# Kernel optimization log

Measured on AMD Instinct MI355X. Metric: run time of the kernel, lower is better.

## Reference

```python
import jax, jax.numpy as jnp
import numpy as np

B, H, S, D = 8, 16, 512, 512  # note: module's final matmul requires D == S


def setup_inputs() -> dict:
    key = jax.random.key(0)
    kq, kk, kv = jax.random.split(key, 3)
    q = jax.random.normal(kq, (B, H, S, D), dtype=jnp.float32)
    k = jax.random.normal(kk, (B, H, S, D), dtype=jnp.float32)
    v = jax.random.normal(kv, (B, H, S, D), dtype=jnp.float32)
    return {"q": q, "k": k, "v": v}


def reference(q, k, v):
    # scaled = (q @ k^T) / sqrt(d_k); mask path is unreachable in the original
    scale = 1.0 / jnp.sqrt(jnp.asarray(q.shape[-1], dtype=q.dtype))
    scores = jax.nn.softmax(scale * jnp.einsum('bhsd,bhtd->bhst', q, k), axis=-1)
    # NOTE: faithful to the original's nonstandard scores @ v^T (not scores @ v)
    out = jnp.einsum('bhst,bhdt->bhsd', scores, v)  # == scores @ v.swapaxes(-2,-1)
    return out
```

## Files before the change

### kernel.cpp

```cpp
#include <hip/hip_runtime.h>
#include <hip/hip_bf16.h>


typedef __attribute__((ext_vector_type(4))) float floatx4;
typedef __attribute__((ext_vector_type(8))) short shortx8;

#define SEQ 512
#define DIM 512
#define MQ   64
#define NTH 512
#define KCH  32
#define LDA 520
#define LDBS 32

__device__ __forceinline__ unsigned short f2bf(float f) {
  union { __hip_bfloat16 b; unsigned short u; } cv;
  cv.b = __float2bfloat16(f);
  return cv.u;
}

__device__ __forceinline__ uint2 cvt4(float4 f) {
  union { __hip_bfloat162 b; unsigned int u; } lo, hi;
  lo.b = __float22bfloat162_rn(make_float2(f.x, f.y));
  hi.b = __float22bfloat162_rn(make_float2(f.z, f.w));
  uint2 r; r.x = lo.u; r.y = hi.u;
  return r;
}

__global__ __launch_bounds__(NTH, 1)
void sdpa_kernel(const float* __restrict__ q, const float* __restrict__ k,
                 const float* __restrict__ v, float* __restrict__ out) {
  __shared__ unsigned short smA[MQ * LDA];
  __shared__ unsigned short smB[2][SEQ * LDBS];
  __shared__ float red[MQ][4];

  const int tid  = threadIdx.x;
  const int lane = tid & 63;
  const int wid  = tid >> 6;
  const int strip = wid >> 1;
  const int half  = wid & 1;
  const int l15  = lane & 15;
  const int quad = lane >> 4;

  const int id = blockIdx.x;
  const int cx = id & 7;
  const int g  = id >> 3;
  const int qtile = g & 7;
  const int head  = ((g >> 3) << 3) | cx;

  const size_t hb = (size_t)head * (SEQ * DIM);
  const float* qh = q + hb + (size_t)qtile * MQ * DIM;
  const float* kh = k + hb;
  const float* vh = v + hb;
  float*       oh = out + hb + (size_t)qtile * MQ * DIM;

  const float scale = 0.044194173824159216f;

  const int r0 = tid >> 3;
  const int c4 = tid & 7;
  const int sldx = r0 * LDBS + ((c4 ^ (r0 & 6)) << 2);

  float4 rv[8];

  #pragma unroll
  for (int i = 0; i < 8; ++i)
    rv[i] = *(const float4*)(kh + (size_t)(i * 64 + r0) * DIM + (c4 << 2));

  {
    const int qc  = tid & 127;
    const int qr0 = tid >> 7;
    #pragma unroll
    for (int i = 0; i < 16; ++i) {
      int row = i * 4 + qr0;
      float4 f = *(const float4*)(qh + (size_t)row * DIM + (qc << 2));
      f.x *= scale; f.y *= scale; f.z *= scale; f.w *= scale;
      *(uint2*)(&smA[row * LDA + (qc << 2)]) = cvt4(f);
    }
  }

  #pragma unroll
  for (int i = 0; i < 8; ++i)
    *(uint2*)(&smB[0][i * 64 * LDBS + sldx]) = cvt4(rv[i]);
  __syncthreads();

  floatx4 acc[16];
  #pragma unroll
  for (int i = 0; i < 16; ++i) acc[i] = (floatx4)(0.0f);

  const int arow = (strip * 16 + l15) * LDA + quad * 8;
  const int bu = (((quad << 1) ^ (l15 & 6)) << 2);

  int cur = 0;
  for (int kc = 0; kc < 16; ++kc) {
    const float* src = (kc < 15) ? (kh + (kc + 1) * KCH) : vh;
    #pragma unroll
    for (int i = 0; i < 8; ++i)
      rv[i] = *(const float4*)(src + (size_t)(i * 64 + r0) * DIM + (c4 << 2));

    shortx8 a = *(const shortx8*)(&smA[arow + kc * KCH]);
    #pragma unroll
    for (int ct = 0; ct < 16; ++ct) {
      int brow = half * 256 + ct * 16 + l15;
      shortx8 b = *(const shortx8*)(&smB[cur][brow * LDBS + bu]);
      acc[ct] = __builtin_amdgcn_mfma_f32_16x16x32_bf16(a, b, acc[ct], 0, 0, 0);
    }
    __builtin_amdgcn_sched_barrier(0);
    #pragma unroll
    for (int i = 0; i < 8; ++i)
      *(uint2*)(&smB[cur ^ 1][i * 64 * LDBS + sldx]) = cvt4(rv[i]);
    __syncthreads();
    cur ^= 1;
  }

  float mx[4], sm[4];
  #pragma unroll
  for (int r = 0; r < 4; ++r) mx[r] = -1e30f;
  #pragma unroll
  for (int ct = 0; ct < 16; ++ct)
    #pragma unroll
    for (int r = 0; r < 4; ++r) mx[r] = fmaxf(mx[r], acc[ct][r]);
  #pragma unroll
  for (int off = 8; off >= 1; off >>= 1)
    #pragma unroll
    for (int r = 0; r < 4; ++r) mx[r] = fmaxf(mx[r], __shfl_xor(mx[r], off, 16));

  const int row0 = strip * 16 + quad * 4;
  if (l15 == 0) {
    #pragma unroll
    for (int r = 0; r < 4; ++r) red[row0 + r][half] = mx[r];
  }
  __syncthreads();
  #pragma unroll
  for (int r = 0; r < 4; ++r) {
    mx[r] = fmaxf(red[row0 + r][0], red[row0 + r][1]);
    sm[r] = 0.0f;
  }
  #pragma unroll
  for (int ct = 0; ct < 16; ++ct)
    #pragma unroll
    for (int r = 0; r < 4; ++r) {
      float e = __expf(acc[ct][r] - mx[r]);
      acc[ct][r] = e;
      sm[r] += e;
    }
  #pragma unroll
  for (int off = 8; off >= 1; off >>= 1)
    #pragma unroll
    for (int r = 0; r < 4; ++r) sm[r] += __shfl_xor(sm[r], off, 16);
  if (l15 == 0) {
    #pragma unroll
    for (int r = 0; r < 4; ++r) red[row0 + r][2 + half] = sm[r];
  }
  __syncthreads();
  float inv[4];
  #pragma unroll
  for (int r = 0; r < 4; ++r) inv[r] = 1.0f / (red[row0 + r][2] + red[row0 + r][3]);

  #pragma unroll
  for (int ct = 0; ct < 16; ++ct) {
    int t = half * 256 + ct * 16 + l15;
    #pragma unroll
    for (int r = 0; r < 4; ++r) {
      smA[(row0 + r) * LDA + t] = f2bf(acc[ct][r] * inv[r]);
    }
  }
  __syncthreads();

  #pragma unroll
  for (int i = 0; i < 16; ++i) acc[i] = (floatx4)(0.0f);

  for (int tc = 0; tc < 16; ++tc) {
    if (tc < 15) {
      #pragma unroll
      for (int i = 0; i < 8; ++i)
        rv[i] = *(const float4*)(vh + (size_t)(i * 64 + r0) * DIM
                                 + (tc + 1) * KCH + (c4 << 2));
    }
    shortx8 a = *(const shortx8*)(&smA[arow + tc * KCH]);
    #pragma unroll
    for (int dt = 0; dt < 16; ++dt) {
      int brow = half * 256 + dt * 16 + l15;
      shortx8 b = *(const shortx8*)(&smB[cur][brow * LDBS + bu]);
      acc[dt] = __builtin_amdgcn_mfma_f32_16x16x32_bf16(a, b, acc[dt], 0, 0, 0);
    }
    if (tc < 15) {
      __builtin_amdgcn_sched_barrier(0);
      #pragma unroll
      for (int i = 0; i < 8; ++i)
        *(uint2*)(&smB[cur ^ 1][i * 64 * LDBS + sldx]) = cvt4(rv[i]);
      __syncthreads();
      cur ^= 1;
    }
  }

  #pragma unroll
  for (int dt = 0; dt < 16; ++dt) {
    int col = half * 256 + dt * 16 + l15;
    #pragma unroll
    for (int r = 0; r < 4; ++r) {
      oh[(row0 + r) * DIM + col] = acc[dt][r];
    }
  }
}

extern "C" void kernel_launch(void* const* d_in, const int* in_sizes, int n_in,
                              void* d_out, int out_size, void* d_ws, size_t ws_size,
                              hipStream_t stream) {
  const float* q = (const float*)d_in[0];
  const float* k = (const float*)d_in[1];
  const float* v = (const float*)d_in[2];
  float* out = (float*)d_out;
  (void)in_sizes; (void)n_in; (void)out_size; (void)d_ws; (void)ws_size;
  sdpa_kernel<<<dim3(8 * 16 * (SEQ / MQ)), dim3(NTH), 0, stream>>>(q, k, v, out);
}
```

Baseline: 549.8 us.

## Double waves per block and deepen the global prefetch to two chunks

The block grows from 8 to 16 waves. Each wave now owns a 16-row strip and a quarter of the key or feature columns, so it holds 8 accumulator tiles instead of 16. The row max and row sum reductions in the softmax now combine four partial values per row instead of two. A STEP macro with two alternating register buffers keeps global loads two chunks ahead, and the K and V loops share one 32-step schedule. This aims to add latency hiding and spread MFMA work across more waves, at the cost of more barrier participants and a launch-bounds hint that may cap registers hard enough to cause spills.

```diff
diff --git a/kernel.cpp b/kernel.cpp
--- a/kernel.cpp
+++ b/kernel.cpp
@@ -8,7 +8,7 @@
 #define SEQ 512
 #define DIM 512
 #define MQ   64
-#define NTH 512
+#define NTH 1024
 #define KCH  32
 #define LDA 520
 #define LDBS 32
@@ -27,18 +27,18 @@
   return r;
 }
 
-__global__ __launch_bounds__(NTH, 1)
+__global__ __launch_bounds__(NTH, 4)
 void sdpa_kernel(const float* __restrict__ q, const float* __restrict__ k,
                  const float* __restrict__ v, float* __restrict__ out) {
   __shared__ unsigned short smA[MQ * LDA];
   __shared__ unsigned short smB[2][SEQ * LDBS];
-  __shared__ float red[MQ][4];
+  __shared__ float red[MQ][8];
 
   const int tid  = threadIdx.x;
   const int lane = tid & 63;
   const int wid  = tid >> 6;
-  const int strip = wid >> 1;
-  const int half  = wid & 1;
+  const int strip = wid >> 2;
+  const int qcol  = wid & 3;
   const int l15  = lane & 15;
   const int quad = lane >> 4;
 
@@ -60,18 +60,18 @@
   const int c4 = tid & 7;
   const int sldx = r0 * LDBS + ((c4 ^ (r0 & 6)) << 2);
 
-  float4 rv[8];
-
-  #pragma unroll
-  for (int i = 0; i < 8; ++i)
-    rv[i] = *(const float4*)(kh + (size_t)(i * 64 + r0) * DIM + (c4 << 2));
+  float4 rvA[4], rvB[4];
+
+  #pragma unroll
+  for (int i = 0; i < 4; ++i)
+    rvA[i] = *(const float4*)(kh + (size_t)(i * 128 + r0) * DIM + (c4 << 2));
 
   {
     const int qc  = tid & 127;
     const int qr0 = tid >> 7;
     #pragma unroll
-    for (int i = 0; i < 16; ++i) {
-      int row = i * 4 + qr0;
+    for (int i = 0; i < 8; ++i) {
+      int row = i * 8 + qr0;
       float4 f = *(const float4*)(qh + (size_t)row * DIM + (qc << 2));
       f.x *= scale; f.y *= scale; f.z *= scale; f.w *= scale;
       *(uint2*)(&smA[row * LDA + (qc << 2)]) = cvt4(f);
@@ -79,44 +79,57 @@
   }
 
   #pragma unroll
-  for (int i = 0; i < 8; ++i)
-    *(uint2*)(&smB[0][i * 64 * LDBS + sldx]) = cvt4(rv[i]);
-  __syncthreads();
-
-  floatx4 acc[16];
-  #pragma unroll
-  for (int i = 0; i < 16; ++i) acc[i] = (floatx4)(0.0f);
+  for (int i = 0; i < 4; ++i)
+    *(uint2*)(&smB[0][i * 128 * LDBS + sldx]) = cvt4(rvA[i]);
+  #pragma unroll
+  for (int i = 0; i < 4; ++i)
+    rvA[i] = *(const float4*)(kh + KCH + (size_t)(i * 128 + r0) * DIM + (c4 << 2));
+  __syncthreads();
+
+  floatx4 acc[8];
+  #pragma unroll
+  for (int i = 0; i < 8; ++i) acc[i] = (floatx4)(0.0f);
 
   const int arow = (strip * 16 + l15) * LDA + quad * 8;
   const int bu = (((quad << 1) ^ (l15 & 6)) << 2);
-
   int cur = 0;
-  for (int kc = 0; kc < 16; ++kc) {
-    const float* src = (kc < 15) ? (kh + (kc + 1) * KCH) : vh;
-    #pragma unroll
-    for (int i = 0; i < 8; ++i)
-      rv[i] = *(const float4*)(src + (size_t)(i * 64 + r0) * DIM + (c4 << 2));
-
-    shortx8 a = *(const shortx8*)(&smA[arow + kc * KCH]);
-    #pragma unroll
-    for (int ct = 0; ct < 16; ++ct) {
-      int brow = half * 256 + ct * 16 + l15;
-      shortx8 b = *(const shortx8*)(&smB[cur][brow * LDBS + bu]);
-      acc[ct] = __builtin_amdgcn_mfma_f32_16x16x32_bf16(a, b, acc[ct], 0, 0, 0);
-    }
-    __builtin_amdgcn_sched_barrier(0);
-    #pragma unroll
-    for (int i = 0; i < 8; ++i)
-      *(uint2*)(&smB[cur ^ 1][i * 64 * LDBS + sldx]) = cvt4(rv[i]);
-    __syncthreads();
-    cur ^= 1;
+
+  #define STEP(cc, RD, WR)                                                      \
+  {                                                                             \
+    if ((cc) + 2 < 32) {                                                        \
+      const float* s_ = ((cc) + 2 < 16) ? (kh + ((cc) + 2) * KCH)               \
+                                        : (vh + ((cc) - 14) * KCH);             \
+      _Pragma("unroll")                                                         \
+      for (int i = 0; i < 4; ++i)                                               \
+        WR[i] = *(const float4*)(s_ + (size_t)(i * 128 + r0) * DIM + (c4 << 2));\
+    }                                                                           \
+    shortx8 a_ = *(const shortx8*)(&smA[arow + ((cc) & 15) * KCH]);             \
+    _Pragma("unroll")                                                           \
+    for (int t_ = 0; t_ < 8; ++t_) {                                            \
+      int brow_ = qcol * 128 + t_ * 16 + l15;                                   \
+      shortx8 b_ = *(const shortx8*)(&smB[cur][brow_ * LDBS + bu]);             \
+      acc[t_] = __builtin_amdgcn_mfma_f32_16x16x32_bf16(a_, b_, acc[t_], 0,0,0);\
+    }                                                                           \
+    if ((cc) + 1 < 32) {                                                        \
+      __builtin_amdgcn_sched_barrier(0);     \
+      _Pragma("unroll")                                                         \
+      for (int i = 0; i < 4; ++i)                                               \
+        *(uint2*)(&smB[cur ^ 1][i * 128 * LDBS + sldx]) = cvt4(RD[i]);          \
+      __syncthreads();                                                          \
+      cur ^= 1;                                                                 \
+    }                                                                           \
+  }
+
+  for (int kc = 0; kc < 16; kc += 2) {
+    STEP(kc,     rvA, rvB);
+    STEP(kc + 1, rvB, rvA);
   }
 
   float mx[4], sm[4];
   #pragma unroll
   for (int r = 0; r < 4; ++r) mx[r] = -1e30f;
   #pragma unroll
-  for (int ct = 0; ct < 16; ++ct)
+  for (int ct = 0; ct < 8; ++ct)
     #pragma unroll
     for (int r = 0; r < 4; ++r) mx[r] = fmaxf(mx[r], acc[ct][r]);
   #pragma unroll
@@ -127,16 +140,17 @@
   const int row0 = strip * 16 + quad * 4;
   if (l15 == 0) {
     #pragma unroll
-    for (int r = 0; r < 4; ++r) red[row0 + r][half] = mx[r];
+    for (int r = 0; r < 4; ++r) red[row0 + r][qcol] = mx[r];
   }
   __syncthreads();
   #pragma unroll
   for (int r = 0; r < 4; ++r) {
-    mx[r] = fmaxf(red[row0 + r][0], red[row0 + r][1]);
+    mx[r] = fmaxf(fmaxf(red[row0 + r][0], red[row0 + r][1]),
+                  fmaxf(red[row0 + r][2], red[row0 + r][3]));
     sm[r] = 0.0f;
   }
   #pragma unroll
-  for (int ct = 0; ct < 16; ++ct)
+  for (int ct = 0; ct < 8; ++ct)
     #pragma unroll
     for (int r = 0; r < 4; ++r) {
       float e = __expf(acc[ct][r] - mx[r]);
@@ -149,16 +163,18 @@
     for (int r = 0; r < 4; ++r) sm[r] += __shfl_xor(sm[r], off, 16);
   if (l15 == 0) {
     #pragma unroll
-    for (int r = 0; r < 4; ++r) red[row0 + r][2 + half] = sm[r];
+    for (int r = 0; r < 4; ++r) red[row0 + r][4 + qcol] = sm[r];
   }
   __syncthreads();
   float inv[4];
   #pragma unroll
-  for (int r = 0; r < 4; ++r) inv[r] = 1.0f / (red[row0 + r][2] + red[row0 + r][3]);
-
-  #pragma unroll
-  for (int ct = 0; ct < 16; ++ct) {
-    int t = half * 256 + ct * 16 + l15;
+  for (int r = 0; r < 4; ++r)
+    inv[r] = 1.0f / (red[row0 + r][4] + red[row0 + r][5] +
+                     red[row0 + r][6] + red[row0 + r][7]);
+
+  #pragma unroll
+  for (int ct = 0; ct < 8; ++ct) {
+    int t = qcol * 128 + ct * 16 + l15;
     #pragma unroll
     for (int r = 0; r < 4; ++r) {
       smA[(row0 + r) * LDA + t] = f2bf(acc[ct][r] * inv[r]);
@@ -167,35 +183,16 @@
   __syncthreads();
 
   #pragma unroll
-  for (int i = 0; i < 16; ++i) acc[i] = (floatx4)(0.0f);
-
-  for (int tc = 0; tc < 16; ++tc) {
-    if (tc < 15) {
-      #pragma unroll
-      for (int i = 0; i < 8; ++i)
-        rv[i] = *(const float4*)(vh + (size_t)(i * 64 + r0) * DIM
-                                 + (tc + 1) * KCH + (c4 << 2));
-    }
-    shortx8 a = *(const shortx8*)(&smA[arow + tc * KCH]);
-    #pragma unroll
-    for (int dt = 0; dt < 16; ++dt) {
-      int brow = half * 256 + dt * 16 + l15;
-      shortx8 b = *(const shortx8*)(&smB[cur][brow * LDBS + bu]);
-      acc[dt] = __builtin_amdgcn_mfma_f32_16x16x32_bf16(a, b, acc[dt], 0, 0, 0);
-    }
-    if (tc < 15) {
-      __builtin_amdgcn_sched_barrier(0);
-      #pragma unroll
-      for (int i = 0; i < 8; ++i)
-        *(uint2*)(&smB[cur ^ 1][i * 64 * LDBS + sldx]) = cvt4(rv[i]);
-      __syncthreads();
-      cur ^= 1;
-    }
-  }
-
-  #pragma unroll
-  for (int dt = 0; dt < 16; ++dt) {
-    int col = half * 256 + dt * 16 + l15;
+  for (int i = 0; i < 8; ++i) acc[i] = (floatx4)(0.0f);
+
+  for (int tc = 16; tc < 32; tc += 2) {
+    STEP(tc,     rvA, rvB);
+    STEP(tc + 1, rvB, rvA);
+  }
+
+  #pragma unroll
+  for (int dt = 0; dt < 8; ++dt) {
+    int col = qcol * 128 + dt * 16 + l15;
     #pragma unroll
     for (int r = 0; r < 4; ++r) {
       oh[(row0 + r) * DIM + col] = acc[dt][r];
```

After: 681.2 us. 1.24x slower.
